# Performance work log

Measured on AMD Instinct MI355X. Metric: run time of the kernel, lower is better.

The kernel has to match this reference:

```python
import jax, jax.numpy as jnp
import numpy as np

HIDDEN = 300      # hidden_dim (char embedding dim / conv in-channels)
N_LETTERS = 128   # letters_dim (vocab of characters)
NUM_FILTERS = 30  # number of conv blocks; each outputs HIDDEN//NUM_FILTERS channels
KSIZE = 3
MAX_WLEN = 16     # max word length in chars
N_WORDS = 16384   # number of words in the batch


def setup_inputs() -> dict:
    key = jax.random.key(0)
    k1, k2, k3, k4 = jax.random.split(key, 4)
    words_batch = jax.random.randint(k1, (MAX_WLEN, N_WORDS), 0, N_LETTERS)  # [L, N]
    emb_table = jax.random.normal(k2, (N_LETTERS, HIDDEN), dtype=jnp.float32)
    # 30 convs of shape [HIDDEN//30, HIDDEN, 3] stacked along out-channels -> one [HIDDEN, HIDDEN, 3]
    fan_in = HIDDEN * KSIZE
    conv_w = jax.random.normal(k3, (HIDDEN, HIDDEN, KSIZE), dtype=jnp.float32) / np.float32(np.sqrt(fan_in))
    conv_b = jax.random.normal(k4, (HIDDEN,), dtype=jnp.float32) * 0.01
    return {"words_batch": words_batch, "emb_table": emb_table, "conv_w": conv_w, "conv_b": conv_b}


def reference(words_batch, emb_table, conv_w, conv_b):
    # embedding lookup: [L, N] -> [L, N, D]
    x = emb_table[words_batch]
    # transpose(0,1).transpose(1,2): [L, N, D] -> [N, D, L]
    x = jnp.transpose(x, (1, 2, 0))
    # 30 independent Conv1d(D -> D//30, k=3, pad=1) concatenated over out-channels
    # == single Conv1d(D -> D, k=3, pad=1) with stacked weights (max-over-time is per-channel)
    y = jax.lax.conv_general_dilated(
        x, conv_w,
        window_strides=(1,), padding=[(1, 1)],
        dimension_numbers=("NCH", "OIH", "NCH"),
    )
    y = jax.nn.relu(y + conv_b[None, :, None])  # [N, D, L]; dropout is identity (eval / keep_prob=1)
    # temporal max pool per channel, then concat over the 30 blocks == per-channel max
    return jnp.max(y, axis=2)  # [N, D]
```

## Files before the change

kernel.cpp:

```cpp
#include <hip/hip_runtime.h>
#include <hip/hip_fp16.h>

#define N_WORDS   16384
#define MAX_WLEN  16
#define HIDDEN    300
#define N_LETTERS 128
#define KSIZE     3

#define TLET   129
#define TPAD   304
#define CH8    38
#define THREADS_TOTAL (N_WORDS * CH8)

#define WT_FLOATS  (HIDDEN * HIDDEN * KSIZE)
#define WT_BYTES   (WT_FLOATS * 4)
#define T16_HALFS  (3 * TLET * TPAD)
#define T16_BYTES  (T16_HALFS * 2)

__global__ __launch_bounds__(256) void transpose_w(
    const float* __restrict__ in,
    float* __restrict__ out)
{
    __shared__ float tile[64][65];
    const int bx = blockIdx.x * 64;
    const int by = blockIdx.y * 64;
    const int tx = threadIdx.x & 63;
    const int ty = threadIdx.x >> 6;

    #pragma unroll
    for (int r = ty; r < 64; r += 4) {
        const int row = by + r, col = bx + tx;
        tile[r][tx] = (row < HIDDEN && col < HIDDEN * KSIZE)
                          ? in[row * (HIDDEN * KSIZE) + col] : 0.0f;
    }
    __syncthreads();
    #pragma unroll
    for (int r = ty; r < 64; r += 4) {
        const int row = bx + r, col = by + tx;
        if (row < HIDDEN * KSIZE && col < HIDDEN)
            out[row * HIDDEN + col] = tile[tx][r];
    }
}

__global__ __launch_bounds__(320) void precompute_fp16(
    const float* __restrict__ emb,
    const float* __restrict__ wt,
    __half* __restrict__ T16)
{
    __shared__ float emb_s[HIDDEN];
    const int c = blockIdx.x;
    const int k = blockIdx.y;
    const int o = threadIdx.x;
    __half* __restrict__ row_out = T16 + ((size_t)k * TLET + c) * TPAD;

    if (c == N_LETTERS) {
        if (o < TPAD) row_out[o] = __float2half(0.0f);
        return;
    }

    if (o < HIDDEN) emb_s[o] = emb[c * HIDDEN + o];
    __syncthreads();

    if (o >= HIDDEN) {
        if (o < TPAD) row_out[o] = __float2half(0.0f);
        return;
    }

    float s = 0.0f;
    const float* __restrict__ base = wt + k * HIDDEN + o;
    #pragma unroll 12
    for (int i = 0; i < HIDDEN; ++i)
        s = fmaf(emb_s[i], base[i * (3 * HIDDEN)], s);
    row_out[o] = __float2half(s);
}

union H8 { uint4 u; __half2 h2[4]; };

__global__ __launch_bounds__(256) void conv_gather_f16(
    const int*    __restrict__ words,
    const __half* __restrict__ T16,
    const float*  __restrict__ bias,
    float*        __restrict__ out)
{
    const unsigned g   = blockIdx.x * 256u + threadIdx.x;
    const unsigned n   = g / CH8;
    const unsigned ch8 = g % CH8;

    int c[MAX_WLEN + 2];
    c[0] = N_LETTERS;
    c[MAX_WLEN + 1] = N_LETTERS;
    #pragma unroll
    for (int l = 0; l < MAX_WLEN; ++l)
        c[l + 1] = words[l * N_WORDS + n];

    const __half* __restrict__ T0 = T16;
    const __half* __restrict__ T1 = T16 + (size_t)TLET * TPAD;
    const __half* __restrict__ T2 = T16 + (size_t)2 * TLET * TPAD;
    const unsigned cho = ch8 * 8;

    float m[8];
    #pragma unroll
    for (int j = 0; j < 8; ++j) m[j] = -1e30f;

    #pragma unroll
    for (int l = 0; l < MAX_WLEN; ++l) {
        H8 a, b, d;
        a.u = *(const uint4*)(T0 + (unsigned)c[l]     * TPAD + cho);
        b.u = *(const uint4*)(T1 + (unsigned)c[l + 1] * TPAD + cho);
        d.u = *(const uint4*)(T2 + (unsigned)c[l + 2] * TPAD + cho);
        #pragma unroll
        for (int j = 0; j < 4; ++j) {
            const float2 fa = __half22float2(a.h2[j]);
            const float2 fb = __half22float2(b.h2[j]);
            const float2 fd = __half22float2(d.h2[j]);
            m[2 * j]     = fmaxf(m[2 * j],     fa.x + fb.x + fd.x);
            m[2 * j + 1] = fmaxf(m[2 * j + 1], fa.y + fb.y + fd.y);
        }
    }

    const float4* __restrict__ bias4 = (const float4*)bias;
    float4* __restrict__ out4 = (float4*)(out + (size_t)n * HIDDEN) + ch8 * 2;
    const bool tail = (ch8 == CH8 - 1);

    const float4 b0 = bias4[ch8 * 2];
    float4 r0;
    r0.x = fmaxf(m[0] + b0.x, 0.0f);
    r0.y = fmaxf(m[1] + b0.y, 0.0f);
    r0.z = fmaxf(m[2] + b0.z, 0.0f);
    r0.w = fmaxf(m[3] + b0.w, 0.0f);
    out4[0] = r0;

    if (!tail) {
        const float4 b1 = bias4[ch8 * 2 + 1];
        float4 r1;
        r1.x = fmaxf(m[4] + b1.x, 0.0f);
        r1.y = fmaxf(m[5] + b1.y, 0.0f);
        r1.z = fmaxf(m[6] + b1.z, 0.0f);
        r1.w = fmaxf(m[7] + b1.w, 0.0f);
        out4[1] = r1;
    }
}

extern "C" void kernel_launch(void* const* d_in, const int* in_sizes, int n_in,
                              void* d_out, int out_size, void* d_ws, size_t ws_size,
                              hipStream_t stream) {
    const int*   words = (const int*)  d_in[0];
    const float* emb   = (const float*)d_in[1];
    const float* w     = (const float*)d_in[2];
    const float* bias  = (const float*)d_in[3];
    float*       out   = (float*)d_out;

    float*  wt  = (float*)d_ws;
    __half* T16 = (__half*)((char*)d_ws + WT_BYTES);

    dim3 tgrid((HIDDEN * KSIZE + 63) / 64, (HIDDEN + 63) / 64);
    transpose_w<<<tgrid, 256, 0, stream>>>(w, wt);

    dim3 pgrid(TLET, KSIZE);
    precompute_fp16<<<pgrid, 320, 0, stream>>>(emb, wt, T16);

    const int blocks = THREADS_TOTAL / 256;
    conv_gather_f16<<<blocks, 256, 0, stream>>>(words, T16, bias, out);
}
```

Baseline: 112.6 us.

## Stage per-slice lookup tables in LDS and peel padding steps in gather

The gather kernel now copies a 10-chunk channel slice of the three letter-by-channel fp16 tables into shared memory. Each block then processes 64 words for that slice from LDS instead of reading the tables from global or L2 memory. The first and last time steps are peeled so the zero padding row is no longer needed. The weight transpose now writes bf16 in a k-major layout to make the precompute reads coalesced. The bf16 weights add rounding error, and every block pays a table-load cost plus one barrier.

```diff
diff --git a/kernel.cpp b/kernel.cpp
--- a/kernel.cpp
+++ b/kernel.cpp
@@ -7,19 +7,29 @@
 #define N_LETTERS 128
 #define KSIZE     3
 
-#define TLET   129
-#define TPAD   304
+#define RPAD   304
 #define CH8    38
-#define THREADS_TOTAL (N_WORDS * CH8)
-
-#define WT_FLOATS  (HIDDEN * HIDDEN * KSIZE)
-#define WT_BYTES   (WT_FLOATS * 4)
-#define T16_HALFS  (3 * TLET * TPAD)
-#define T16_BYTES  (T16_HALFS * 2)
-
-__global__ __launch_bounds__(256) void transpose_w(
+#define TROWS  N_LETTERS
+
+#define WTB_ELEMS (HIDDEN * KSIZE * RPAD)
+#define WTB_BYTES (WTB_ELEMS * 2)
+
+#define NCH_SL   10
+#define W_BLK    64
+#define GTHREADS 640
+
+__device__ __forceinline__ float bf16_to_f32(unsigned short h) {
+    union { unsigned int u; float f; } v; v.u = ((unsigned int)h) << 16; return v.f;
+}
+__device__ __forceinline__ unsigned short f32_to_bf16(float f) {
+    union { float f; unsigned int u; } v; v.f = f;
+    const unsigned int r = v.u + 0x7fffu + ((v.u >> 16) & 1u);
+    return (unsigned short)(r >> 16);
+}
+
+__global__ __launch_bounds__(256) void transpose_w_bf16(
     const float* __restrict__ in,
-    float* __restrict__ out)
+    unsigned short* __restrict__ out)
 {
     __shared__ float tile[64][65];
     const int bx = blockIdx.x * 64;
@@ -36,78 +46,99 @@
     __syncthreads();
     #pragma unroll
     for (int r = ty; r < 64; r += 4) {
-        const int row = bx + r, col = by + tx;
-        if (row < HIDDEN * KSIZE && col < HIDDEN)
-            out[row * HIDDEN + col] = tile[tx][r];
-    }
-}
-
-__global__ __launch_bounds__(320) void precompute_fp16(
+        const int ik = bx + r, o = by + tx;
+        if (ik < HIDDEN * KSIZE && o < HIDDEN) {
+            const int i = ik / 3, k = ik % 3;
+            out[((size_t)k * HIDDEN + i) * RPAD + o] = f32_to_bf16(tile[tx][r]);
+        }
+    }
+}
+
+__global__ __launch_bounds__(320) void precompute_f16(
     const float* __restrict__ emb,
-    const float* __restrict__ wt,
+    const unsigned short* __restrict__ wtb,
     __half* __restrict__ T16)
 {
     __shared__ float emb_s[HIDDEN];
     const int c = blockIdx.x;
     const int k = blockIdx.y;
     const int o = threadIdx.x;
-    __half* __restrict__ row_out = T16 + ((size_t)k * TLET + c) * TPAD;
-
-    if (c == N_LETTERS) {
-        if (o < TPAD) row_out[o] = __float2half(0.0f);
-        return;
-    }
+    __half* __restrict__ row_out = T16 + ((size_t)k * TROWS + c) * RPAD;
 
     if (o < HIDDEN) emb_s[o] = emb[c * HIDDEN + o];
     __syncthreads();
 
     if (o >= HIDDEN) {
-        if (o < TPAD) row_out[o] = __float2half(0.0f);
+        if (o < RPAD) row_out[o] = __float2half(0.0f);
         return;
     }
 
     float s = 0.0f;
-    const float* __restrict__ base = wt + k * HIDDEN + o;
-    #pragma unroll 12
+    const unsigned short* __restrict__ base = wtb + (size_t)k * HIDDEN * RPAD + o;
+    #pragma unroll 10
     for (int i = 0; i < HIDDEN; ++i)
-        s = fmaf(emb_s[i], base[i * (3 * HIDDEN)], s);
+        s = fmaf(emb_s[i], bf16_to_f32(base[i * RPAD]), s);
     row_out[o] = __float2half(s);
 }
 
 union H8 { uint4 u; __half2 h2[4]; };
 
-__global__ __launch_bounds__(256) void conv_gather_f16(
+__global__ __launch_bounds__(GTHREADS) void conv_gather_lds(
     const int*    __restrict__ words,
     const __half* __restrict__ T16,
     const float*  __restrict__ bias,
     float*        __restrict__ out)
 {
-    const unsigned g   = blockIdx.x * 256u + threadIdx.x;
-    const unsigned n   = g / CH8;
-    const unsigned ch8 = g % CH8;
-
-    int c[MAX_WLEN + 2];
-    c[0] = N_LETTERS;
-    c[MAX_WLEN + 1] = N_LETTERS;
+    __shared__ __align__(16) __half sl[3 * TROWS * NCH_SL * 8];
+    const int s   = blockIdx.y;
+    const int wg  = blockIdx.x;
+    const int off = (s < 3) ? s * NCH_SL : 28;
+
+    {
+        const uint4* __restrict__ src = (const uint4*)T16;
+        uint4* __restrict__ dst = (uint4*)sl;
+        #pragma unroll
+        for (int i = threadIdx.x; i < 3 * TROWS * NCH_SL; i += GTHREADS) {
+            const int row = i / NCH_SL;
+            const int ch  = i - row * NCH_SL;
+            dst[i] = src[row * (RPAD / 8) + off + ch];
+        }
+    }
+    __syncthreads();
+
+    const int item = threadIdx.x;
+    const int wloc = item / NCH_SL;
+    const int ch   = item - wloc * NCH_SL;
+    const int ch8  = off + ch;
+    const int n    = wg * W_BLK + wloc;
+
+    int c[MAX_WLEN];
     #pragma unroll
     for (int l = 0; l < MAX_WLEN; ++l)
-        c[l + 1] = words[l * N_WORDS + n];
-
-    const __half* __restrict__ T0 = T16;
-    const __half* __restrict__ T1 = T16 + (size_t)TLET * TPAD;
-    const __half* __restrict__ T2 = T16 + (size_t)2 * TLET * TPAD;
-    const unsigned cho = ch8 * 8;
+        c[l] = words[l * N_WORDS + n];
+
+    const __half* __restrict__ S = sl + ch * 8;
+    #define LD(k_, c_) (*(const uint4*)(S + ((k_) * TROWS + (c_)) * (NCH_SL * 8)))
 
     float m[8];
-    #pragma unroll
-    for (int j = 0; j < 8; ++j) m[j] = -1e30f;
-
-    #pragma unroll
-    for (int l = 0; l < MAX_WLEN; ++l) {
+    {
+        H8 b, d;
+        b.u = LD(1, c[0]);
+        d.u = LD(2, c[1]);
+        #pragma unroll
+        for (int j = 0; j < 4; ++j) {
+            const float2 fb = __half22float2(b.h2[j]);
+            const float2 fd = __half22float2(d.h2[j]);
+            m[2 * j]     = fb.x + fd.x;
+            m[2 * j + 1] = fb.y + fd.y;
+        }
+    }
+    #pragma unroll
+    for (int l = 1; l < MAX_WLEN - 1; ++l) {
         H8 a, b, d;
-        a.u = *(const uint4*)(T0 + (unsigned)c[l]     * TPAD + cho);
-        b.u = *(const uint4*)(T1 + (unsigned)c[l + 1] * TPAD + cho);
-        d.u = *(const uint4*)(T2 + (unsigned)c[l + 2] * TPAD + cho);
+        a.u = LD(0, c[l - 1]);
+        b.u = LD(1, c[l]);
+        d.u = LD(2, c[l + 1]);
         #pragma unroll
         for (int j = 0; j < 4; ++j) {
             const float2 fa = __half22float2(a.h2[j]);
@@ -117,10 +148,22 @@
             m[2 * j + 1] = fmaxf(m[2 * j + 1], fa.y + fb.y + fd.y);
         }
     }
+    {
+        H8 a, b;
+        a.u = LD(0, c[MAX_WLEN - 2]);
+        b.u = LD(1, c[MAX_WLEN - 1]);
+        #pragma unroll
+        for (int j = 0; j < 4; ++j) {
+            const float2 fa = __half22float2(a.h2[j]);
+            const float2 fb = __half22float2(b.h2[j]);
+            m[2 * j]     = fmaxf(m[2 * j],     fa.x + fb.x);
+            m[2 * j + 1] = fmaxf(m[2 * j + 1], fa.y + fb.y);
+        }
+    }
+    #undef LD
 
     const float4* __restrict__ bias4 = (const float4*)bias;
     float4* __restrict__ out4 = (float4*)(out + (size_t)n * HIDDEN) + ch8 * 2;
-    const bool tail = (ch8 == CH8 - 1);
 
     const float4 b0 = bias4[ch8 * 2];
     float4 r0;
@@ -130,7 +173,7 @@
     r0.w = fmaxf(m[3] + b0.w, 0.0f);
     out4[0] = r0;
 
-    if (!tail) {
+    if (ch8 != CH8 - 1) {
         const float4 b1 = bias4[ch8 * 2 + 1];
         float4 r1;
         r1.x = fmaxf(m[4] + b1.x, 0.0f);
@@ -150,15 +193,15 @@
     const float* bias  = (const float*)d_in[3];
     float*       out   = (float*)d_out;
 
-    float*  wt  = (float*)d_ws;
-    __half* T16 = (__half*)((char*)d_ws + WT_BYTES);
+    unsigned short* wtb = (unsigned short*)d_ws;
+    __half*         T16 = (__half*)((char*)d_ws + WTB_BYTES);
 
     dim3 tgrid((HIDDEN * KSIZE + 63) / 64, (HIDDEN + 63) / 64);
-    transpose_w<<<tgrid, 256, 0, stream>>>(w, wt);
-
-    dim3 pgrid(TLET, KSIZE);
-    precompute_fp16<<<pgrid, 320, 0, stream>>>(emb, wt, T16);
-
-    const int blocks = THREADS_TOTAL / 256;
-    conv_gather_f16<<<blocks, 256, 0, stream>>>(words, T16, bias, out);
-}
+    transpose_w_bf16<<<tgrid, 256, 0, stream>>>(w, wtb);
+
+    dim3 pgrid(N_LETTERS, KSIZE);
+    precompute_f16<<<pgrid, 320, 0, stream>>>(emb, wtb, T16);
+
+    dim3 ggrid(N_WORDS / W_BLK, 4);
+    conv_gather_lds<<<ggrid, GTHREADS, 0, stream>>>(words, T16, bias, out);
+}
```

Result: faster. 107.9 us (-4.1%).
